# Kernel tuning notes

Measured on AMD Instinct MI355X. Metric: run time of the kernel, lower is better.

## Reference

```python
import jax, jax.numpy as jnp
import numpy as np

B, N, C, T = 512, 62, 8, 64
K = 8          # topk
HEADS = 4
OUT = 128
EPS = 1e-5     # BatchNorm1d eps
NEG_SLOPE = 0.2  # GATConv leaky_relu slope


def _gat(x, W, a_src, a_dst, bias, src, dst, valid, num_nodes, concat):
    """PyG GATConv (eval mode, self-loops already in edge list)."""
    H, Co = a_src.shape[1], a_src.shape[2]
    xl = (x @ W.T).reshape(num_nodes, H, Co)          # [V,H,Co]
    al_src = jnp.sum(xl * a_src, axis=-1)             # [V,H]
    al_dst = jnp.sum(xl * a_dst, axis=-1)             # [V,H]
    alpha = jax.nn.leaky_relu(al_src[src] + al_dst[dst], NEG_SLOPE)  # [E,H]
    alpha = jnp.where(valid[:, None], alpha, -jnp.inf)
    amax = jax.ops.segment_max(alpha, dst, num_segments=num_nodes)   # [V,H]
    ex = jnp.where(valid[:, None], jnp.exp(alpha - amax[dst]), 0.0)
    denom = jax.ops.segment_sum(ex, dst, num_segments=num_nodes)     # [V,H]
    w = ex / denom[dst]                                              # softmax per dst
    out = jax.ops.segment_sum(xl[src] * w[:, :, None], dst, num_segments=num_nodes)
    out = out.reshape(num_nodes, H * Co) if concat else out.mean(axis=1)
    return out + bias


def reference(x, edge_index, W1, W2, b_sp, V_sp, bn_w, bn_b,
              g1_w, g1_asrc, g1_adst, g1_b, g2_w, g2_asrc, g2_adst, g2_b):
    # edge_index is unused: spatial=True rebuilds the graph from attention.
    x4 = x.reshape(B, N, C, T)
    # SpatialAttention: ((x @ W1) @ W2) -> tanh(. @ V + b) -> BatchNorm1d(N)
    prod = jnp.einsum('bnct,t->bnc', x4, W1) @ W2      # [B,N,N]
    S = jnp.tanh(prod @ V_sp + b_sp)                   # [B,N,N]
    mean = S.mean(axis=(0, 2), keepdims=True)          # BN over channel dim 1
    var = S.var(axis=(0, 2), keepdims=True)
    adj = (S - mean) / jnp.sqrt(var + EPS) * bn_w[None, :, None] + bn_b[None, :, None]
    # topk mask + dense_to_sparse: exactly K edges per (batch, row)
    _, idx = jax.lax.top_k(adj, K)                     # [B,N,K] column indices
    offs = (jnp.arange(B) * N)[:, None, None]
    src = (jnp.broadcast_to(jnp.arange(N)[None, :, None], (B, N, K)) + offs).reshape(-1)
    dst = (idx + offs).reshape(-1)
    # GATConv: remove_self_loops then add_self_loops -> mask topk self-edges, append loops
    loops = jnp.arange(B * N)
    valid = jnp.concatenate([src != dst, jnp.ones(B * N, dtype=bool)])
    src = jnp.concatenate([src, loops])
    dst = jnp.concatenate([dst, loops])
    h = x4.reshape(B * N, C * T)
    h = jax.nn.relu(_gat(h, g1_w, g1_asrc, g1_adst, g1_b, src, dst, valid, B * N, True))
    h = jax.nn.relu(_gat(h, g2_w, g2_asrc, g2_adst, g2_b, src, dst, valid, B * N, False))
    return h


def setup_inputs() -> dict:
    key = jax.random.key(0)
    ks = jax.random.split(key, 16)
    d_in = C * T  # 512
    return {
        'x': jax.random.normal(ks[0], (B, N, C, T), jnp.float32),
        'edge_index': jax.random.randint(ks[1], (2, 128), 0, B * N, jnp.int64) if False else jax.random.randint(ks[1], (2, 128), 0, B * N).astype(jnp.int32),
        'W1': jax.random.uniform(ks[2], (T,), jnp.float32),
        'W2': jax.random.normal(ks[3], (C, N), jnp.float32) * 0.1,
        'b_sp': jax.random.normal(ks[4], (1, N, N), jnp.float32) * 0.1,
        'V_sp': jax.random.normal(ks[5], (N, N), jnp.float32) * 0.1,
        'bn_w': jnp.ones((N,), jnp.float32),
        'bn_b': jnp.zeros((N,), jnp.float32),
        'g1_w': jax.random.normal(ks[6], (HEADS * OUT, d_in), jnp.float32) * 0.04,
        'g1_asrc': jax.random.normal(ks[7], (1, HEADS, OUT), jnp.float32) * 0.06,
        'g1_adst': jax.random.normal(ks[8], (1, HEADS, OUT), jnp.float32) * 0.06,
        'g1_b': jnp.zeros((HEADS * OUT,), jnp.float32),
        'g2_w': jax.random.normal(ks[9], (HEADS * OUT, HEADS * OUT), jnp.float32) * 0.04,
        'g2_asrc': jax.random.normal(ks[10], (1, HEADS, OUT), jnp.float32) * 0.06,
        'g2_adst': jax.random.normal(ks[11], (1, HEADS, OUT), jnp.float32) * 0.06,
        'g2_b': jnp.zeros((OUT,), jnp.float32),
    }
```

## Files before the change

### kernel.cpp

```cpp
#include <hip/hip_runtime.h>
#include <math.h>

#define B_ 512
#define N_ 62
#define V_ (B_ * N_)
#define TOPK_ 8

typedef __attribute__((ext_vector_type(8))) short bf16x8;
typedef __attribute__((ext_vector_type(4))) float f32x4;

__device__ __forceinline__ unsigned short bf16rn(float f) {
    unsigned int u = __float_as_uint(f);
    unsigned int r = (u + 0x7fffu + ((u >> 16) & 1u)) >> 16;
    return (unsigned short)r;
}
__device__ __forceinline__ float bf16tof(unsigned short h) {
    return __uint_as_float(((unsigned int)h) << 16);
}

__device__ __forceinline__ void gload16(const void* g, void* l) {
    __builtin_amdgcn_global_load_lds(
        (const __attribute__((address_space(1))) unsigned int*)g,
        (__attribute__((address_space(3))) unsigned int*)l, 16, 0, 0);
}

__global__ __launch_bounds__(64) void spatial_S(
    const float* __restrict__ x, const float* __restrict__ W1,
    const float* __restrict__ W2, const float* __restrict__ bsp,
    const float* __restrict__ Vsp, float* __restrict__ S,
    unsigned short* __restrict__ A2)
{
    int blk = blockIdx.x;
    int n = blk % N_;
    int lane = threadIdx.x;
    const float* xr = x + (size_t)blk * 512;
    float w1 = W1[lane];

    float y[8];
#pragma unroll
    for (int c = 0; c < 8; ++c) {
        float xv = xr[c * 64 + lane];
        A2[(size_t)blk * 512 + c * 64 + lane] = bf16rn(xv);
        float p = xv * w1;
#pragma unroll
        for (int off = 32; off; off >>= 1) p += __shfl_xor(p, off);
        y[c] = p;
    }

    __shared__ float pr[N_];
    if (lane < N_) {
        float acc = 0.f;
#pragma unroll
        for (int c = 0; c < 8; ++c) acc += y[c] * W2[c * N_ + lane];
        pr[lane] = acc;
    }
    __syncthreads();
    if (lane < N_) {
        float acc = bsp[n * N_ + lane];
        for (int k = 0; k < N_; ++k) acc += pr[k] * Vsp[k * N_ + lane];
        S[(size_t)blk * N_ + lane] = tanhf(acc);
    }
}

__global__ __launch_bounds__(256) void bn_part(
    const float* __restrict__ S, double* __restrict__ part)
{
    int n = blockIdx.x >> 4, slice = blockIdx.x & 15;
    double s = 0.0, s2 = 0.0;
    int i0 = slice * 1984;
    for (int i = i0 + threadIdx.x; i < i0 + 1984; i += 256) {
        int b = i / N_, m = i - b * N_;
        float v = S[((size_t)b * N_ + n) * N_ + m];
        s += v; s2 += (double)v * v;
    }
    __shared__ double sh[256], sh2[256];
    sh[threadIdx.x] = s; sh2[threadIdx.x] = s2;
    __syncthreads();
    for (int off = 128; off; off >>= 1) {
        if (threadIdx.x < off) {
            sh[threadIdx.x] += sh[threadIdx.x + off];
            sh2[threadIdx.x] += sh2[threadIdx.x + off];
        }
        __syncthreads();
    }
    if (threadIdx.x == 0) {
        part[((size_t)n * 16 + slice) * 2 + 0] = sh[0];
        part[((size_t)n * 16 + slice) * 2 + 1] = sh2[0];
    }
}

__global__ __launch_bounds__(64) void bn_final(
    const double* __restrict__ part, const float* __restrict__ bnw,
    const float* __restrict__ bnb, float* __restrict__ scale,
    float* __restrict__ shift)
{
    int n = threadIdx.x;
    if (n >= N_) return;
    double s = 0.0, s2 = 0.0;
    for (int j = 0; j < 16; ++j) {
        s  += part[((size_t)n * 16 + j) * 2 + 0];
        s2 += part[((size_t)n * 16 + j) * 2 + 1];
    }
    const double cnt = (double)(B_ * N_);
    double mean = s / cnt;
    double var = s2 / cnt - mean * mean;
    float inv = (float)(1.0 / sqrt(var + 1e-5));
    scale[n] = bnw[n] * inv;
    shift[n] = bnb[n] - (float)mean * bnw[n] * inv;
}

__global__ __launch_bounds__(64) void topk_mask(
    const float* __restrict__ S, const float* __restrict__ scale,
    const float* __restrict__ shift, unsigned long long* __restrict__ maskT)
{
    int blk = blockIdx.x;
    int b = blk / N_, n = blk - b * N_;
    int lane = threadIdx.x;
    float v = (lane < N_) ? S[(size_t)blk * N_ + lane] * scale[n] + shift[n]
                          : -INFINITY;
    bool sel = false;
#pragma unroll
    for (int k = 0; k < TOPK_; ++k) {
        float mv = v; int mi = lane;
#pragma unroll
        for (int off = 32; off; off >>= 1) {
            float ov = __shfl_xor(mv, off);
            int   oi = __shfl_xor(mi, off);
            if (ov > mv || (ov == mv && oi < mi)) { mv = ov; mi = oi; }
        }
        if (lane == mi) { sel = true; v = -INFINITY; }
    }
    unsigned long long row = __ballot(sel) | (1ull << n);
    if (lane < N_ && ((row >> lane) & 1ull))
        atomicOr(&maskT[(size_t)b * N_ + lane], 1ull << n);
}

__global__ __launch_bounds__(256) void zero_u64(unsigned long long* p, int n)
{
    int i = blockIdx.x * 256 + threadIdx.x;
    if (i < n) p[i] = 0ull;
}

__global__ __launch_bounds__(256) void split_pair(
    const float* __restrict__ in, unsigned short* __restrict__ out, int total4)
{
    int gid = blockIdx.x * 256 + threadIdx.x;
    if (gid >= total4) return;
    int row = gid >> 7;
    int c = (gid & 127) * 4;
    float4 v = ((const float4*)in)[gid];
    ushort4 h, l;
    float f;
    h.x = bf16rn(v.x); f = v.x - bf16tof(h.x); l.x = bf16rn(f);
    h.y = bf16rn(v.y); f = v.y - bf16tof(h.y); l.y = bf16rn(f);
    h.z = bf16rn(v.z); f = v.z - bf16tof(h.z); l.z = bf16rn(f);
    h.w = bf16rn(v.w); f = v.w - bf16tof(h.w); l.w = bf16rn(f);
    *(ushort4*)(&out[(size_t)row * 1024 + c])       = h;
    *(ushort4*)(&out[(size_t)row * 1024 + 512 + c]) = l;
}

__global__ __launch_bounds__(256) void gemm_bf16(
    const unsigned short* __restrict__ Ah, const unsigned short* __restrict__ Bw,
    unsigned short* __restrict__ Cs)
{
    __shared__ __align__(16) unsigned short smem[16384];
    char* As = (char*)smem;
    char* Bs = (char*)(smem + 8192);

    int tid = threadIdx.x;
    int lane = tid & 63, w = tid >> 6;

    int flat = blockIdx.y * 4 + blockIdx.x;
    int swz = (flat & 7) * 124 + (flat >> 3);
    int by = swz >> 2, bx = swz & 3;
    int bm = by * 128, bn = bx * 128;

    int wr = w >> 1, wc = w & 1;

    f32x4 acc[4][4];
#pragma unroll
    for (int mf = 0; mf < 4; ++mf)
#pragma unroll
        for (int nf = 0; nf < 4; ++nf) acc[mf][nf] = (f32x4){0.f, 0.f, 0.f, 0.f};

    int srow = w * 8 + (lane >> 3);
    int kcol = (lane & 7) ^ (lane >> 3);
    int ldsoff = w * 1024;

    for (int kt = 0; kt < 16; ++kt) {
        int k0 = (kt & 7) * 64;
        int bBase = (kt >> 3) * 512 + k0;
#pragma unroll
        for (int i = 0; i < 4; ++i) {
            int row = i * 32 + srow;
            gload16(Ah + (size_t)(bm + row) * 512 + k0 + kcol * 8,
                    As + i * 4096 + ldsoff);
            gload16(Bw + (size_t)(bn + row) * 1024 + bBase + kcol * 8,
                    Bs + i * 4096 + ldsoff);
        }
        __syncthreads();

#pragma unroll
        for (int kk = 0; kk < 2; ++kk) {
            bf16x8 af[4], bfr[4];
#pragma unroll
            for (int mf = 0; mf < 4; ++mf)
                af[mf] = *(const bf16x8*)(As + (wr*64 + mf*16 + (lane&15))*128
                                             + ((kk*4 + (lane>>4)) ^ (lane&7))*16);
#pragma unroll
            for (int nf = 0; nf < 4; ++nf)
                bfr[nf] = *(const bf16x8*)(Bs + (wc*64 + nf*16 + (lane&15))*128
                                              + ((kk*4 + (lane>>4)) ^ (lane&7))*16);
#pragma unroll
            for (int mf = 0; mf < 4; ++mf)
#pragma unroll
                for (int nf = 0; nf < 4; ++nf)
                    acc[mf][nf] = __builtin_amdgcn_mfma_f32_16x16x32_bf16(
                        af[mf], bfr[nf], acc[mf][nf], 0, 0, 0);
        }
        __syncthreads();
    }

    int r0 = bm + wr * 64 + (lane >> 4) * 4;
    int c0 = bn + wc * 64 + (lane & 15);
#pragma unroll
    for (int mf = 0; mf < 4; ++mf)
#pragma unroll
        for (int nf = 0; nf < 4; ++nf)
#pragma unroll
            for (int r = 0; r < 4; ++r) {
                float v = acc[mf][nf][r];
                unsigned short h = bf16rn(v);
                unsigned short l = bf16rn(v - bf16tof(h));
                size_t row = (size_t)(r0 + mf * 16 + r);
                Cs[row * 1024 + c0 + nf * 16] = h;
                Cs[row * 1024 + 512 + c0 + nf * 16] = l;
            }
}

template <int APPLY>
__global__ __launch_bounds__(512, 4) void gat_aggM(
    const unsigned short* __restrict__ XL,
    const float* __restrict__ asrc, const float* __restrict__ adst,
    const unsigned long long* __restrict__ maskT,
    const float* __restrict__ bias,
    unsigned short* __restrict__ H)
{
    __shared__ __align__(16) char lds[34816];
    float* shs = (float*)(lds + 32768);
    float* shd = (float*)(lds + 33760);

    int b = blockIdx.x;
    int tid = threadIdx.x;
    int lane = tid & 63, w = tid >> 6;
    const unsigned short* base = XL + (size_t)b * N_ * 1024;

    for (int t = w; t < 248; t += 8) {
        int s = t >> 2, h = t & 3;
        const unsigned short* xv = base + (size_t)s * 1024 + h * 128;
        float x0 = bf16tof(xv[lane])      + bf16tof(xv[512 + lane]);
        float x1 = bf16tof(xv[64 + lane]) + bf16tof(xv[576 + lane]);
        float ps = x0 * asrc[h * 128 + lane] + x1 * asrc[h * 128 + 64 + lane];
        float pd = x0 * adst[h * 128 + lane] + x1 * adst[h * 128 + 64 + lane];
#pragma unroll
        for (int off = 32; off; off >>= 1) {
            ps += __shfl_xor(ps, off);
            pd += __shfl_xor(pd, off);
        }
        if (lane == 0) { shs[t] = ps; shd[t] = pd; }
    }
    __syncthreads();

    for (int t = w; t < 248; t += 8) {
        int d = t >> 2, h = t & 3;
        unsigned long long m = maskT[(size_t)b * N_ + d];
        bool valid = (lane < N_) && ((m >> lane) & 1ull);
        float a = -INFINITY;
        if (valid) {
            float raw = shs[lane * 4 + h] + shd[d * 4 + h];
            a = (raw > 0.f) ? raw : 0.2f * raw;
        }
        float mx = a;
#pragma unroll
        for (int off = 32; off; off >>= 1) mx = fmaxf(mx, __shfl_xor(mx, off));
        float ex = valid ? expf(a - mx) : 0.f;
        float sm = ex;
#pragma unroll
        for (int off = 32; off; off >>= 1) sm += __shfl_xor(sm, off);
        float wv = valid ? ex / sm : 0.f;
        int addr = h * 8192 + d * 128
                 + (((lane >> 3) ^ (d & 7)) << 4) + ((lane & 7) << 1);
        *(unsigned short*)(lds + addr) = bf16rn(wv);
    }
    __syncthreads();

    int cc = lane & 15, lh = lane >> 4;

    union U8 { unsigned short s[8]; bf16x8 v; };

#pragma unroll
    for (int ch = 0; ch < 4; ++ch) {
        f32x4 acc[4];
#pragma unroll
        for (int mf = 0; mf < 4; ++mf) acc[mf] = (f32x4){0.f, 0.f, 0.f, 0.f};

        const unsigned short* xp = base + (size_t)(lh * 8) * 1024
                                        + ch * 128 + w * 16 + cc;
#pragma unroll
        for (int kk = 0; kk < 2; ++kk) {
            U8 bh, bl;
#pragma unroll
            for (int j = 0; j < 8; ++j) {
                size_t o = (size_t)(kk * 32 + j) * 1024;
                bh.s[j] = xp[o];
                bl.s[j] = xp[o + 512];
            }
            bf16x8 af[4];
#pragma unroll
            for (int mf = 0; mf < 4; ++mf)
                af[mf] = *(const bf16x8*)(lds + ch * 8192
                              + (mf * 16 + cc) * 128
                              + (((kk * 4 + lh) ^ (cc & 7)) << 4));
#pragma unroll
            for (int mf = 0; mf < 4; ++mf) {
                acc[mf] = __builtin_amdgcn_mfma_f32_16x16x32_bf16(
                    af[mf], bh.v, acc[mf], 0, 0, 0);
                acc[mf] = __builtin_amdgcn_mfma_f32_16x16x32_bf16(
                    af[mf], bl.v, acc[mf], 0, 0, 0);
            }
        }

        int c = ch * 128 + w * 16 + cc;
        float bc = APPLY ? bias[c] : 0.f;
#pragma unroll
        for (int mf = 0; mf < 4; ++mf)
#pragma unroll
            for (int r = 0; r < 4; ++r) {
                int d = mf * 16 + lh * 4 + r;
                if (d < N_) {
                    float v = acc[mf][r] + bc;
                    if (APPLY) v = v > 0.f ? v : 0.f;
                    H[(size_t)(b * N_ + d) * 512 + c] = bf16rn(v);
                }
            }
    }
}

__global__ __launch_bounds__(512) void mean_relu(
    const unsigned short* __restrict__ H2, const float* __restrict__ bias,
    float* __restrict__ out)
{
    int tid = threadIdx.x;
    int v = blockIdx.x * 4 + (tid >> 7);
    int c = tid & 127;
    const unsigned short* t = H2 + (size_t)v * 512;
    float s = bf16tof(t[c]) + bf16tof(t[128 + c]) +
              bf16tof(t[256 + c]) + bf16tof(t[384 + c]);
    s = s * 0.25f + bias[c];
    out[(size_t)v * 128 + c] = s > 0.f ? s : 0.f;
}

extern "C" void kernel_launch(void* const* d_in, const int* in_sizes, int n_in,
                              void* d_out, int out_size, void* d_ws, size_t ws_size,
                              hipStream_t stream)
{
    const float* x    = (const float*)d_in[0];
    const float* W1   = (const float*)d_in[2];
    const float* W2   = (const float*)d_in[3];
    const float* bsp  = (const float*)d_in[4];
    const float* Vsp  = (const float*)d_in[5];
    const float* bnw  = (const float*)d_in[6];
    const float* bnb  = (const float*)d_in[7];
    const float* g1w  = (const float*)d_in[8];
    const float* g1as = (const float*)d_in[9];
    const float* g1ad = (const float*)d_in[10];
    const float* g1b  = (const float*)d_in[11];
    const float* g2w  = (const float*)d_in[12];
    const float* g2as = (const float*)d_in[13];
    const float* g2ad = (const float*)d_in[14];
    const float* g2b  = (const float*)d_in[15];
    float* out = (float*)d_out;

    char* ws = (char*)d_ws;
    size_t off = 0;
    auto alloc = [&](size_t bytes) -> void* {
        void* p = ws + off;
        off += (bytes + 255) & ~(size_t)255;
        return p;
    };
    float* S      = (float*)alloc((size_t)V_ * N_ * 4);
    float* scale  = (float*)alloc(N_ * 4);
    float* shift  = (float*)alloc(N_ * 4);
    double* part  = (double*)alloc((size_t)N_ * 16 * 2 * 8);
    unsigned long long* maskT = (unsigned long long*)alloc((size_t)V_ * 8);
    unsigned short* A2  = (unsigned short*)alloc((size_t)V_ * 512 * 2);
    unsigned short* Bw1 = (unsigned short*)alloc((size_t)512 * 1024 * 2);
    unsigned short* Bw2 = (unsigned short*)alloc((size_t)512 * 1024 * 2);
    unsigned short* XL  = (unsigned short*)alloc((size_t)(V_ + 2) * 1024 * 2);
    unsigned short* H1  = (unsigned short*)alloc((size_t)V_ * 512 * 2);
    unsigned short* H2  = (unsigned short*)alloc((size_t)V_ * 512 * 2);

    zero_u64<<<(V_ + 255) / 256, 256, 0, stream>>>(maskT, V_);
    spatial_S<<<V_, 64, 0, stream>>>(x, W1, W2, bsp, Vsp, S, A2);
    bn_part<<<N_ * 16, 256, 0, stream>>>(S, part);
    bn_final<<<1, 64, 0, stream>>>(part, bnw, bnb, scale, shift);
    topk_mask<<<V_, 64, 0, stream>>>(S, scale, shift, maskT);

    split_pair<<<(512 * 128 + 255) / 256, 256, 0, stream>>>(g1w, Bw1, 512 * 128);
    split_pair<<<(512 * 128 + 255) / 256, 256, 0, stream>>>(g2w, Bw2, 512 * 128);

    dim3 gg(4, 248);
    gemm_bf16<<<gg, 256, 0, stream>>>(A2, Bw1, XL);
    gat_aggM<1><<<B_, 512, 0, stream>>>(XL, g1as, g1ad, maskT, g1b, H1);

    gemm_bf16<<<gg, 256, 0, stream>>>(H1, Bw2, XL);
    gat_aggM<0><<<B_, 512, 0, stream>>>(XL, g2as, g2ad, maskT, g2b, H2);
    mean_relu<<<V_ / 4, 512, 0, stream>>>(H2, g2b, out);
}
```

Before: 407.6 us.

## Fuse head-mean and ReLU into second GAT aggregation; vectorize attention logits

The second GAT aggregation now accumulates the four head outputs in registers and writes the averaged, biased, ReLU'd float output directly. This removes the H2 intermediate buffer and the separate mean_relu launch. The per-node attention logit computation is rewritten so each thread handles a 64-element slice with 16-byte vector loads against attention vectors staged in LDS, replacing the wave-per-(node,head) shuffle reductions. The launch-bounds occupancy hint drops from 4 to 2 blocks. Precision changes slightly, because the head mean is now taken in fp32 before any bf16 rounding.

```diff
diff --git a/kernel.cpp b/kernel.cpp
--- a/kernel.cpp
+++ b/kernel.cpp
@@ -239,35 +239,53 @@
 }
 
 template <int APPLY>
-__global__ __launch_bounds__(512, 4) void gat_aggM(
+__global__ __launch_bounds__(512, 2) void gat_aggM(
     const unsigned short* __restrict__ XL,
     const float* __restrict__ asrc, const float* __restrict__ adst,
     const unsigned long long* __restrict__ maskT,
     const float* __restrict__ bias,
-    unsigned short* __restrict__ H)
-{
-    __shared__ __align__(16) char lds[34816];
-    float* shs = (float*)(lds + 32768);
-    float* shd = (float*)(lds + 33760);
+    void* __restrict__ outp)
+{
+    __shared__ __align__(16) char lds[38976];
+    float* av  = (float*)(lds + 32768);
+    float* dv  = (float*)(lds + 34848);
+    float* shs = (float*)(lds + 36928);
+    float* shd = (float*)(lds + 37952);
 
     int b = blockIdx.x;
     int tid = threadIdx.x;
     int lane = tid & 63, w = tid >> 6;
     const unsigned short* base = XL + (size_t)b * N_ * 1024;
 
-    for (int t = w; t < 248; t += 8) {
-        int s = t >> 2, h = t & 3;
-        const unsigned short* xv = base + (size_t)s * 1024 + h * 128;
-        float x0 = bf16tof(xv[lane])      + bf16tof(xv[512 + lane]);
-        float x1 = bf16tof(xv[64 + lane]) + bf16tof(xv[576 + lane]);
-        float ps = x0 * asrc[h * 128 + lane] + x1 * asrc[h * 128 + 64 + lane];
-        float pd = x0 * adst[h * 128 + lane] + x1 * adst[h * 128 + 64 + lane];
-#pragma unroll
-        for (int off = 32; off; off >>= 1) {
-            ps += __shfl_xor(ps, off);
-            pd += __shfl_xor(pd, off);
-        }
-        if (lane == 0) { shs[t] = ps; shd[t] = pd; }
+    av[(tid >> 6) * 65 + (tid & 63)] = asrc[tid];
+    dv[(tid >> 6) * 65 + (tid & 63)] = adst[tid];
+    __syncthreads();
+
+    {
+        int s = tid >> 3, sl = tid & 7;
+        const unsigned short* xp = base + (size_t)s * 1024 + sl * 64;
+        float ps = 0.f, pd = 0.f;
+        union V8 { uint4 u; unsigned short s[8]; };
+#pragma unroll
+        for (int g = 0; g < 8; ++g) {
+            V8 vh, vl;
+            vh.u = *(const uint4*)(xp + g * 8);
+            vl.u = *(const uint4*)(xp + 512 + g * 8);
+            const float* avp = av + sl * 65 + g * 8;
+            const float* dvp = dv + sl * 65 + g * 8;
+#pragma unroll
+            for (int j = 0; j < 8; ++j) {
+                float xv = bf16tof(vh.s[j]) + bf16tof(vl.s[j]);
+                ps += xv * avp[j];
+                pd += xv * dvp[j];
+            }
+        }
+        ps += __shfl_xor(ps, 1);
+        pd += __shfl_xor(pd, 1);
+        if ((sl & 1) == 0) {
+            shs[s * 4 + (sl >> 1)] = ps;
+            shd[s * 4 + (sl >> 1)] = pd;
+        }
     }
     __syncthreads();
 
@@ -298,6 +316,12 @@
 
     union U8 { unsigned short s[8]; bf16x8 v; };
 
+    f32x4 macc[4];
+    if (APPLY == 0) {
+#pragma unroll
+        for (int mf = 0; mf < 4; ++mf) macc[mf] = (f32x4){0.f, 0.f, 0.f, 0.f};
+    }
+
 #pragma unroll
     for (int ch = 0; ch < 4; ++ch) {
         f32x4 acc[4];
@@ -330,34 +354,42 @@
             }
         }
 
-        int c = ch * 128 + w * 16 + cc;
-        float bc = APPLY ? bias[c] : 0.f;
+        if (APPLY == 1) {
+            int c = ch * 128 + w * 16 + cc;
+            float bc = bias[c];
+            unsigned short* H = (unsigned short*)outp;
+#pragma unroll
+            for (int mf = 0; mf < 4; ++mf)
+#pragma unroll
+                for (int r = 0; r < 4; ++r) {
+                    int d = mf * 16 + lh * 4 + r;
+                    if (d < N_) {
+                        float v = acc[mf][r] + bc;
+                        v = v > 0.f ? v : 0.f;
+                        H[(size_t)(b * N_ + d) * 512 + c] = bf16rn(v);
+                    }
+                }
+        } else {
+#pragma unroll
+            for (int mf = 0; mf < 4; ++mf) macc[mf] += acc[mf];
+        }
+    }
+
+    if (APPLY == 0) {
+        int c = w * 16 + cc;
+        float bc = bias[c];
+        float* outF = (float*)outp;
 #pragma unroll
         for (int mf = 0; mf < 4; ++mf)
 #pragma unroll
             for (int r = 0; r < 4; ++r) {
                 int d = mf * 16 + lh * 4 + r;
                 if (d < N_) {
-                    float v = acc[mf][r] + bc;
-                    if (APPLY) v = v > 0.f ? v : 0.f;
-                    H[(size_t)(b * N_ + d) * 512 + c] = bf16rn(v);
+                    float v = macc[mf][r] * 0.25f + bc;
+                    outF[(size_t)(b * N_ + d) * 128 + c] = v > 0.f ? v : 0.f;
                 }
             }
     }
-}
-
-__global__ __launch_bounds__(512) void mean_relu(
-    const unsigned short* __restrict__ H2, const float* __restrict__ bias,
-    float* __restrict__ out)
-{
-    int tid = threadIdx.x;
-    int v = blockIdx.x * 4 + (tid >> 7);
-    int c = tid & 127;
-    const unsigned short* t = H2 + (size_t)v * 512;
-    float s = bf16tof(t[c]) + bf16tof(t[128 + c]) +
-              bf16tof(t[256 + c]) + bf16tof(t[384 + c]);
-    s = s * 0.25f + bias[c];
-    out[(size_t)v * 128 + c] = s > 0.f ? s : 0.f;
 }
 
 extern "C" void kernel_launch(void* const* d_in, const int* in_sizes, int n_in,
@@ -398,7 +430,6 @@
     unsigned short* Bw2 = (unsigned short*)alloc((size_t)512 * 1024 * 2);
     unsigned short* XL  = (unsigned short*)alloc((size_t)(V_ + 2) * 1024 * 2);
     unsigned short* H1  = (unsigned short*)alloc((size_t)V_ * 512 * 2);
-    unsigned short* H2  = (unsigned short*)alloc((size_t)V_ * 512 * 2);
 
     zero_u64<<<(V_ + 255) / 256, 256, 0, stream>>>(maskT, V_);
     spatial_S<<<V_, 64, 0, stream>>>(x, W1, W2, bsp, Vsp, S, A2);
@@ -414,6 +445,5 @@
     gat_aggM<1><<<B_, 512, 0, stream>>>(XL, g1as, g1ad, maskT, g1b, H1);
 
     gemm_bf16<<<gg, 256, 0, stream>>>(H1, Bw2, XL);
-    gat_aggM<0><<<B_, 512, 0, stream>>>(XL, g2as, g2ad, maskT, g2b, H2);
-    mean_relu<<<V_ / 4, 512, 0, stream>>>(H2, g2b, out);
-}
+    gat_aggM<0><<<B_, 512, 0, stream>>>(XL, g2as, g2ad, maskT, g2b, out);
+}
```

Result: no change. 415.6 us (+2.0%).
